# Kernel optimization log

Hardware: AMD Instinct MI355X
Metric: run time of the kernel (lower is better)

## Reference

```python
import jax, jax.numpy as jnp
import numpy as np

EMBED_DIM = 1024
NUM_HEADS = 16
HEAD_DIM = EMBED_DIM // NUM_HEADS
SCALE = HEAD_DIM ** -0.5


def setup_inputs() -> dict:
    key = jax.random.key(0)
    k1, k2, k3, k4 = jax.random.split(key, 4)
    B, N, C = 4, 2048, EMBED_DIM
    x = jax.random.normal(k1, (B, N, C), dtype=jnp.float32)
    # qkv: Linear(C, 3C, bias=False)
    w_qkv = jax.random.normal(k2, (3 * C, C), dtype=jnp.float32) * (C ** -0.5)
    # proj: Linear(C, C, bias=True)
    w_proj = jax.random.normal(k3, (C, C), dtype=jnp.float32) * (C ** -0.5)
    b_proj = jax.random.normal(k4, (C,), dtype=jnp.float32) * 0.01
    return {"x": x, "w_qkv": w_qkv, "w_proj": w_proj, "b_proj": b_proj}


def reference(x, w_qkv, w_proj, b_proj):
    B, N, C = x.shape
    H, D = NUM_HEADS, HEAD_DIM
    qkv = jnp.einsum('bnc,oc->bno', x, w_qkv)               # [B,N,3C]
    qkv = qkv.reshape(B, N, 3, H, D).transpose(2, 0, 3, 1, 4)  # [3,B,H,N,D]
    q, k, v = qkv[0], qkv[1], qkv[2]
    attn = jnp.einsum('bhnd,bhmd->bhnm', q, k) * SCALE       # [B,H,N,N]
    attn = jax.nn.softmax(attn, axis=-1)
    out = jnp.einsum('bhnm,bhmd->bhnd', attn, v)             # [B,H,N,D]
    out = out.transpose(0, 2, 1, 3).reshape(B, N, C)
    return jnp.einsum('bnc,oc->bno', out, w_proj) + b_proj
```

## Files before the change

### kernel.cpp

```cpp
#include <hip/hip_runtime.h>

#define B_ 4
#define N_ 2048
#define C_ 1024
#define H_ 16
#define D_ 64
#define M_ (B_*N_)

typedef _Float16 f16;
typedef __attribute__((ext_vector_type(2))) _Float16 f16x2;
typedef __attribute__((ext_vector_type(4))) _Float16 f16x4;
typedef __attribute__((ext_vector_type(8))) _Float16 f16x8;
typedef __attribute__((ext_vector_type(4))) float f32x4;
typedef __attribute__((ext_vector_type(16))) float f32x16;
typedef unsigned int u32;
typedef __attribute__((ext_vector_type(2))) u32 u32x2;
typedef __attribute__((ext_vector_type(4))) u32 u32x4;

__device__ __forceinline__ f32x4 mfma16(f16x8 a, f16x8 b, f32x4 c) {
  return __builtin_amdgcn_mfma_f32_16x16x32_f16(a, b, c, 0, 0, 0);
}
__device__ __forceinline__ f32x16 mfma32(f16x8 a, f16x8 b, f32x16 c) {
  return __builtin_amdgcn_mfma_f32_32x32x16_f16(a, b, c, 0, 0, 0);
}

__global__ void cast_f32_f16(const float* __restrict__ in, f16* __restrict__ out,
                             int n4, int scale_n4, float scale) {
  int i = blockIdx.x * blockDim.x + threadIdx.x;
  int stride = gridDim.x * blockDim.x;
  for (; i < n4; i += stride) {
    float4 v = reinterpret_cast<const float4*>(in)[i];
    float s = (i < scale_n4) ? scale : 1.0f;
    f16x4 o = { (f16)(v.x*s), (f16)(v.y*s), (f16)(v.z*s), (f16)(v.w*s) };
    reinterpret_cast<f16x4*>(out)[i] = o;
  }
}

template<int OUTMODE>
__global__ __launch_bounds__(256) void gemm_bt(
    const f16* __restrict__ A, const f16* __restrict__ Bm,
    f16* __restrict__ outH, float* __restrict__ outF,
    const float* __restrict__ bias, int M, int Nn, int K)
{
  __shared__ __align__(16) f16 As[128*32];
  __shared__ __align__(16) f16 Bs[128*32];
  const int tid = threadIdx.x;
  const int lane = tid & 63, wid = tid >> 6;
  const int wr = wid >> 1, wc = wid & 1;
  const int g = lane >> 4, r15 = lane & 15;
  const int nbx = Nn >> 7;
  const int cpx = gridDim.x >> 3;
  const int wg = blockIdx.x;
  const int swz = (wg & 7) * cpx + (wg >> 3);
  const int m0 = (swz / nbx) * 128, n0 = (swz % nbx) * 128;

  f32x4 acc[4][4] = {};

  for (int k0 = 0; k0 < K; k0 += 32) {
#pragma unroll
    for (int i = 0; i < 2; ++i) {
      int chunk = wid*128 + i*64 + lane;
      int row = chunk >> 2, c8 = (chunk & 3) << 3;
      const f16* ga = A  + (size_t)(m0 + row) * K + k0 + c8;
      const f16* gb = Bm + (size_t)(n0 + row) * K + k0 + c8;
      __builtin_amdgcn_global_load_lds(
        (const __attribute__((address_space(1))) unsigned int*)ga,
        (__attribute__((address_space(3))) unsigned int*)&As[(wid*128 + i*64)*8], 16, 0, 0);
      __builtin_amdgcn_global_load_lds(
        (const __attribute__((address_space(1))) unsigned int*)gb,
        (__attribute__((address_space(3))) unsigned int*)&Bs[(wid*128 + i*64)*8], 16, 0, 0);
    }
    __syncthreads();

    f16x8 af[4], bfr[4];
#pragma unroll
    for (int m = 0; m < 4; ++m)
      af[m] = *reinterpret_cast<const f16x8*>(&As[(wr*64 + m*16 + r15)*32 + g*8]);
#pragma unroll
    for (int n = 0; n < 4; ++n)
      bfr[n] = *reinterpret_cast<const f16x8*>(&Bs[(wc*64 + n*16 + r15)*32 + g*8]);
#pragma unroll
    for (int m = 0; m < 4; ++m)
#pragma unroll
      for (int n = 0; n < 4; ++n)
        acc[m][n] = mfma16(af[m], bfr[n], acc[m][n]);
    __syncthreads();
  }

#pragma unroll
  for (int m = 0; m < 4; ++m) {
#pragma unroll
    for (int n = 0; n < 4; ++n) {
#pragma unroll
      for (int r = 0; r < 4; ++r) {
        int row = m0 + wr*64 + m*16 + g*4 + r;
        int col = n0 + wc*64 + n*16 + r15;
        if (OUTMODE == 0) {
          outH[(size_t)row * Nn + col] = (f16)acc[m][n][r];
        } else {
          outF[(size_t)row * Nn + col] = acc[m][n][r] + bias[col];
        }
      }
    }
  }
}

__global__ __launch_bounds__(256) void transpose_v(const f16* __restrict__ qkv,
                                                   f16* __restrict__ vt) {
  __shared__ f16 Ts[64*64];
  const int tid = threadIdx.x;
  const int bh = blockIdx.y, b = bh >> 4, h = bh & 15;
  const int n0 = blockIdx.x * 64;
#pragma unroll
  for (int p = 0; p < 2; ++p) {
    int idx = p*256 + tid;
    int row = idx >> 3, c8 = (idx & 7) << 3;
    f16x8 v = *reinterpret_cast<const f16x8*>(
        qkv + (size_t)(b*N_ + n0 + row)*(3*C_) + 2*C_ + h*D_ + c8);
    *reinterpret_cast<f16x8*>(&Ts[row*64 + c8]) = v;
  }
  __syncthreads();
#pragma unroll
  for (int p = 0; p < 2; ++p) {
    int idx = p*256 + tid;
    int d = idx & 63, cblk = idx >> 6;
    f16x8 o;
#pragma unroll
    for (int j = 0; j < 8; ++j) o[j] = Ts[(cblk*8 + j)*64 + d];
    *reinterpret_cast<f16x8*>(vt + (size_t)(bh*64 + d)*N_ + n0 + cblk*8) = o;
  }
}

__global__ __launch_bounds__(256, 4) void attn_kernel(
    const f16* __restrict__ qkv, const f16* __restrict__ vt,
    f16* __restrict__ attn_out)
{
  __shared__ __align__(16) f16 Ks[2][64*64];
  __shared__ __align__(16) f16 Vs[2][64*64];
  const int tid = threadIdx.x;
  const int lane = tid & 63, w = tid >> 6;
  const int hi = lane >> 5;
  const int r31 = lane & 31;
  const int rm = r31 & 7;
  const int blk = blockIdx.x;
  const int xcd = blk & 7, idx = blk >> 3;
  const int bh = xcd + 8 * (idx >> 4);
  const int bx = idx & 15;
  const int b = bh >> 4, h = bh & 15;
  const int q0 = bx * 128 + w * 32;
  const int RS = 3 * C_;

  f16x8 qf[4];
  {
    const f16* qrow = qkv + (size_t)(b*N_ + q0 + r31) * RS + h*D_;
#pragma unroll
    for (int kk = 0; kk < 4; ++kk)
      qf[kk] = *reinterpret_cast<const f16x8*>(qrow + kk*16 + hi*8);
  }

  f32x16 acc0 = {}, acc1 = {};
  const f16x2 one2 = { (f16)1.0f, (f16)1.0f };
  float la = 0.f, lb = 0.f;

  int cc0 = w*64 + lane, cc1 = 256 + w*64 + lane;
  int R0 = cc0 >> 3, s0_ = (cc0 & 7) ^ (R0 & 7);
  int R1 = cc1 >> 3, s1_ = (cc1 & 7) ^ (R1 & 7);
  const f16* kg0 = qkv + (size_t)(b*N_ + R0) * RS + C_ + h*D_ + s0_*8;
  const f16* kg1 = qkv + (size_t)(b*N_ + R1) * RS + C_ + h*D_ + s1_*8;
  const f16* vg0 = vt + (size_t)(bh*D_ + R0) * N_ + s0_*8;
  const f16* vg1 = vt + (size_t)(bh*D_ + R1) * N_ + s1_*8;

  auto stage = [&](int bufi, int kv0) {
    __builtin_amdgcn_global_load_lds(
      (const __attribute__((address_space(1))) u32*)(kg0 + (size_t)kv0 * RS),
      (__attribute__((address_space(3))) u32*)&Ks[bufi][(w*64)*8], 16, 0, 0);
    __builtin_amdgcn_global_load_lds(
      (const __attribute__((address_space(1))) u32*)(kg1 + (size_t)kv0 * RS),
      (__attribute__((address_space(3))) u32*)&Ks[bufi][(256 + w*64)*8], 16, 0, 0);
    __builtin_amdgcn_global_load_lds(
      (const __attribute__((address_space(1))) u32*)(vg0 + kv0),
      (__attribute__((address_space(3))) u32*)&Vs[bufi][(w*64)*8], 16, 0, 0);
    __builtin_amdgcn_global_load_lds(
      (const __attribute__((address_space(1))) u32*)(vg1 + kv0),
      (__attribute__((address_space(3))) u32*)&Vs[bufi][(256 + w*64)*8], 16, 0, 0);
  };

  int cur = 0;
  stage(0, 0);
  __syncthreads();

  for (int it = 0; it < N_/64; ++it) {
    if (it + 1 < N_/64) stage(cur ^ 1, (it + 1) * 64);
    const f16* KsC = Ks[cur];
    const f16* VsC = Vs[cur];

#pragma unroll
    for (int hh = 0; hh < 2; ++hh) {
      f32x16 T;
      {
        const f32x16 Zc = {};
        __builtin_amdgcn_s_setprio(1);
        int ch = ((hi ^ rm) << 3);
        f16x8 k0 = *reinterpret_cast<const f16x8*>(&KsC[(hh*32 + r31)*64 + ch]);
        T = mfma32(k0, qf[0], Zc);
#pragma unroll
        for (int kk = 1; kk < 4; ++kk) {
          int ch2 = (((kk*2 + hi) ^ rm) << 3);
          f16x8 kx = *reinterpret_cast<const f16x8*>(&KsC[(hh*32 + r31)*64 + ch2]);
          T = mfma32(kx, qf[kk], T);
        }
        __builtin_amdgcn_s_setprio(0);
      }

#pragma unroll
      for (int c2 = 0; c2 < 2; ++c2) {
        float p0 = __builtin_amdgcn_exp2f(T[8*c2 + 0]);
        float p1 = __builtin_amdgcn_exp2f(T[8*c2 + 1]);
        float p2 = __builtin_amdgcn_exp2f(T[8*c2 + 2]);
        float p3 = __builtin_amdgcn_exp2f(T[8*c2 + 3]);
        float p4 = __builtin_amdgcn_exp2f(T[8*c2 + 4]);
        float p5 = __builtin_amdgcn_exp2f(T[8*c2 + 5]);
        float p6 = __builtin_amdgcn_exp2f(T[8*c2 + 6]);
        float p7 = __builtin_amdgcn_exp2f(T[8*c2 + 7]);
        u32 w0 = __builtin_bit_cast(u32, __builtin_amdgcn_cvt_pkrtz(p0, p1));
        u32 w1 = __builtin_bit_cast(u32, __builtin_amdgcn_cvt_pkrtz(p2, p3));
        u32 w2 = __builtin_bit_cast(u32, __builtin_amdgcn_cvt_pkrtz(p4, p5));
        u32 w3 = __builtin_bit_cast(u32, __builtin_amdgcn_cvt_pkrtz(p6, p7));
        la = __builtin_amdgcn_fdot2(__builtin_bit_cast(f16x2, w0), one2, la, false);
        lb = __builtin_amdgcn_fdot2(__builtin_bit_cast(f16x2, w1), one2, lb, false);
        la = __builtin_amdgcn_fdot2(__builtin_bit_cast(f16x2, w2), one2, la, false);
        lb = __builtin_amdgcn_fdot2(__builtin_bit_cast(f16x2, w3), one2, lb, false);

        u32x2 r02 = __builtin_amdgcn_permlane32_swap(w0, w2, false, false);
        u32x2 r13 = __builtin_amdgcn_permlane32_swap(w1, w3, false, false);
        u32x4 fw = { r02[0], r13[0], r02[1], r13[1] };
        f16x8 pf = __builtin_bit_cast(f16x8, fw);

        int c = hh*2 + c2;
        int ch = (((c*2 + hi) ^ rm) << 3);
        f16x8 v0 = *reinterpret_cast<const f16x8*>(&VsC[r31*64 + ch]);
        f16x8 v1 = *reinterpret_cast<const f16x8*>(&VsC[(32 + r31)*64 + ch]);
        __builtin_amdgcn_s_setprio(1);
        acc0 = mfma32(v0, pf, acc0);
        acc1 = mfma32(v1, pf, acc1);
        __builtin_amdgcn_s_setprio(0);
      }
    }

    __syncthreads();
    cur ^= 1;
  }

  float l_own = la + lb;
  float l = l_own + __shfl_xor(l_own, 32);
  float inv = 1.0f / l;
  f16* orow = attn_out + (size_t)(b*N_ + q0 + r31) * C_ + h*D_;
#pragma unroll
  for (int g2 = 0; g2 < 4; ++g2) {
    f16x4 o0, o1;
#pragma unroll
    for (int j = 0; j < 4; ++j) {
      o0[j] = (f16)(acc0[g2*4 + j] * inv);
      o1[j] = (f16)(acc1[g2*4 + j] * inv);
    }
    *reinterpret_cast<f16x4*>(orow + g2*8 + hi*4)      = o0;
    *reinterpret_cast<f16x4*>(orow + 32 + g2*8 + hi*4) = o1;
  }
}

extern "C" void kernel_launch(void* const* d_in, const int* in_sizes, int n_in,
                              void* d_out, int out_size, void* d_ws, size_t ws_size,
                              hipStream_t stream) {
  const float* x      = (const float*)d_in[0];
  const float* w_qkv  = (const float*)d_in[1];
  const float* w_proj = (const float*)d_in[2];
  const float* b_proj = (const float*)d_in[3];
  float* out = (float*)d_out;

  char* ws = (char*)d_ws;
  f16* xb     = (f16*)(ws);
  f16* wqkvb  = (f16*)(ws + 16777216);
  f16* wprojb = (f16*)(ws + 23068672);
  f16* qkvb   = (f16*)(ws + 25165824);
  f16* vtb    = (f16*)(ws + 75497472);
  f16* attnb  = xb;

  cast_f32_f16<<<2048, 256, 0, stream>>>(x,      xb,     (M_*C_)/4, 0, 1.0f);
  cast_f32_f16<<<1024, 256, 0, stream>>>(w_qkv,  wqkvb,  (3*C_*C_)/4, (C_*C_)/4, 0.18033688011112042f);
  cast_f32_f16<<<512,  256, 0, stream>>>(w_proj, wprojb, (C_*C_)/4, 0, 1.0f);

  gemm_bt<0><<<dim3((3*C_/128)*(M_/128)), 256, 0, stream>>>(
      xb, wqkvb, qkvb, nullptr, nullptr, M_, 3*C_, C_);

  transpose_v<<<dim3(N_/64, B_*H_), 256, 0, stream>>>(qkvb, vtb);

  attn_kernel<<<dim3(1024), 256, 0, stream>>>(qkvb, vtb, attnb);

  gemm_bt<1><<<dim3((C_/128)*(M_/128)), 256, 0, stream>>>(
      attnb, wprojb, nullptr, out, b_proj, M_, C_, C_);
}
```

Baseline: 221.8 us.

## Rewrite projection GEMMs with double-buffered LDS, larger tiles and swizzled layout

Replaces the single-buffered 128x128 GEMM with a 512-thread, 128x256-tile kernel that double-buffers 64-wide K slices in LDS. Loads for the next slice are issued before the MFMAs on the current one, synchronised with vmcnt waits and raw barriers. It adds an XOR swizzle on LDS columns to avoid bank conflicts, raises wave priority around the MFMA blocks, and uses supertile block swizzling for L2 reuse. The aim is to hide global-load latency and halve the number of barriers per K step. In exchange, LDS use grows to 96 KB per block and the launch grids are hardcoded, which may limit occupancy.

```diff
diff --git a/kernel.cpp b/kernel.cpp
--- a/kernel.cpp
+++ b/kernel.cpp
@@ -37,55 +37,97 @@
 }
 
 template<int OUTMODE>
-__global__ __launch_bounds__(256) void gemm_bt(
+__global__ __launch_bounds__(512, 2) void gemm_p(
     const f16* __restrict__ A, const f16* __restrict__ Bm,
     f16* __restrict__ outH, float* __restrict__ outF,
-    const float* __restrict__ bias, int M, int Nn, int K)
+    const float* __restrict__ bias, int Nn, int K, int nsup)
 {
-  __shared__ __align__(16) f16 As[128*32];
-  __shared__ __align__(16) f16 Bs[128*32];
+  __shared__ __align__(16) f16 As[2][128*64];
+  __shared__ __align__(16) f16 Bs[2][256*64];
   const int tid = threadIdx.x;
   const int lane = tid & 63, wid = tid >> 6;
-  const int wr = wid >> 1, wc = wid & 1;
+  const int wm = wid >> 2, wn = wid & 3;
   const int g = lane >> 4, r15 = lane & 15;
-  const int nbx = Nn >> 7;
-  const int cpx = gridDim.x >> 3;
-  const int wg = blockIdx.x;
-  const int swz = (wg & 7) * cpx + (wg >> 3);
-  const int m0 = (swz / nbx) * 128, n0 = (swz % nbx) * 128;
+  const int rmod = r15 & 3;
+  const int gx = (g ^ rmod) * 8;
+
+  const int s = blockIdx.x >> 4, w16 = blockIdx.x & 15;
+  const int s_swz = (s & 7) * (2 * nsup) + (s >> 3);
+  const int sm = s_swz / nsup, sn = s_swz % nsup;
+  const int m0 = (sm * 4 + (w16 >> 2)) * 128;
+  const int n0 = (sn * 4 + (w16 & 3)) * 256;
+
+  const int arow = tid >> 2, aslot = tid & 3;
+  const int akc = aslot ^ (arow & 3);
+  const f16* abase  = A  + (size_t)(m0 + arow) * K + akc * 8;
+  const f16* bbase0 = Bm + (size_t)(n0 + arow) * K + akc * 8;
+  const f16* bbase1 = Bm + (size_t)(n0 + arow + 128) * K + akc * 8;
+
+  #define STAGE(buf, kofs, kh)                                                        \
+    do {                                                                              \
+      __builtin_amdgcn_global_load_lds(                                               \
+        (const __attribute__((address_space(1))) u32*)(abase + (kofs) + (kh)*32),     \
+        (__attribute__((address_space(3))) u32*)&As[buf][(kh)*4096 + tid*8], 16,0,0); \
+      __builtin_amdgcn_global_load_lds(                                               \
+        (const __attribute__((address_space(1))) u32*)(bbase0 + (kofs) + (kh)*32),    \
+        (__attribute__((address_space(3))) u32*)&Bs[buf][(kh)*8192 + tid*8], 16,0,0); \
+      __builtin_amdgcn_global_load_lds(                                               \
+        (const __attribute__((address_space(1))) u32*)(bbase1 + (kofs) + (kh)*32),    \
+        (__attribute__((address_space(3))) u32*)&Bs[buf][(kh)*8192 + (tid+512)*8], 16,0,0); \
+    } while (0)
 
   f32x4 acc[4][4] = {};
-
-  for (int k0 = 0; k0 < K; k0 += 32) {
-#pragma unroll
-    for (int i = 0; i < 2; ++i) {
-      int chunk = wid*128 + i*64 + lane;
-      int row = chunk >> 2, c8 = (chunk & 3) << 3;
-      const f16* ga = A  + (size_t)(m0 + row) * K + k0 + c8;
-      const f16* gb = Bm + (size_t)(n0 + row) * K + k0 + c8;
-      __builtin_amdgcn_global_load_lds(
-        (const __attribute__((address_space(1))) unsigned int*)ga,
-        (__attribute__((address_space(3))) unsigned int*)&As[(wid*128 + i*64)*8], 16, 0, 0);
-      __builtin_amdgcn_global_load_lds(
-        (const __attribute__((address_space(1))) unsigned int*)gb,
-        (__attribute__((address_space(3))) unsigned int*)&Bs[(wid*128 + i*64)*8], 16, 0, 0);
+  const int nt = K / 64;
+
+  STAGE(0, 0, 0);
+  STAGE(0, 0, 1);
+
+  int cur = 0;
+  for (int t = 0; t < nt - 1; ++t) {
+#pragma unroll
+    for (int kk = 0; kk < 2; ++kk) {
+      asm volatile("s_waitcnt vmcnt(3)" ::: "memory");
+      __builtin_amdgcn_s_barrier();
+      STAGE(cur ^ 1, (t + 1) * 64, kk);
+      f16x8 af[4], bf[4];
+#pragma unroll
+      for (int m = 0; m < 4; ++m)
+        af[m] = *reinterpret_cast<const f16x8*>(&As[cur][kk*4096 + (wm*64 + m*16 + r15)*32 + gx]);
+#pragma unroll
+      for (int n = 0; n < 4; ++n)
+        bf[n] = *reinterpret_cast<const f16x8*>(&Bs[cur][kk*8192 + (wn*64 + n*16 + r15)*32 + gx]);
+      __builtin_amdgcn_s_setprio(1);
+#pragma unroll
+      for (int m = 0; m < 4; ++m)
+#pragma unroll
+        for (int n = 0; n < 4; ++n)
+          acc[m][n] = mfma16(af[m], bf[n], acc[m][n]);
+      __builtin_amdgcn_s_setprio(0);
     }
-    __syncthreads();
-
-    f16x8 af[4], bfr[4];
+    cur ^= 1;
+  }
+
+#pragma unroll
+  for (int kk = 0; kk < 2; ++kk) {
+    if (kk == 0) asm volatile("s_waitcnt vmcnt(3)" ::: "memory");
+    else         asm volatile("s_waitcnt vmcnt(0)" ::: "memory");
+    __builtin_amdgcn_s_barrier();
+    f16x8 af[4], bf[4];
 #pragma unroll
     for (int m = 0; m < 4; ++m)
-      af[m] = *reinterpret_cast<const f16x8*>(&As[(wr*64 + m*16 + r15)*32 + g*8]);
+      af[m] = *reinterpret_cast<const f16x8*>(&As[cur][kk*4096 + (wm*64 + m*16 + r15)*32 + gx]);
 #pragma unroll
     for (int n = 0; n < 4; ++n)
-      bfr[n] = *reinterpret_cast<const f16x8*>(&Bs[(wc*64 + n*16 + r15)*32 + g*8]);
+      bf[n] = *reinterpret_cast<const f16x8*>(&Bs[cur][kk*8192 + (wn*64 + n*16 + r15)*32 + gx]);
+    __builtin_amdgcn_s_setprio(1);
 #pragma unroll
     for (int m = 0; m < 4; ++m)
 #pragma unroll
       for (int n = 0; n < 4; ++n)
-        acc[m][n] = mfma16(af[m], bfr[n], acc[m][n]);
-    __syncthreads();
-  }
+        acc[m][n] = mfma16(af[m], bf[n], acc[m][n]);
+    __builtin_amdgcn_s_setprio(0);
+  }
+  #undef STAGE
 
 #pragma unroll
   for (int m = 0; m < 4; ++m) {
@@ -93,8 +135,8 @@
     for (int n = 0; n < 4; ++n) {
 #pragma unroll
       for (int r = 0; r < 4; ++r) {
-        int row = m0 + wr*64 + m*16 + g*4 + r;
-        int col = n0 + wc*64 + n*16 + r15;
+        int row = m0 + wm*64 + m*16 + g*4 + r;
+        int col = n0 + wn*64 + n*16 + r15;
         if (OUTMODE == 0) {
           outH[(size_t)row * Nn + col] = (f16)acc[m][n][r];
         } else {
@@ -289,13 +331,13 @@
   cast_f32_f16<<<1024, 256, 0, stream>>>(w_qkv,  wqkvb,  (3*C_*C_)/4, (C_*C_)/4, 0.18033688011112042f);
   cast_f32_f16<<<512,  256, 0, stream>>>(w_proj, wprojb, (C_*C_)/4, 0, 1.0f);
 
-  gemm_bt<0><<<dim3((3*C_/128)*(M_/128)), 256, 0, stream>>>(
-      xb, wqkvb, qkvb, nullptr, nullptr, M_, 3*C_, C_);
+  gemm_p<0><<<dim3(768), 512, 0, stream>>>(
+      xb, wqkvb, qkvb, nullptr, nullptr, 3*C_, C_, 3);
 
   transpose_v<<<dim3(N_/64, B_*H_), 256, 0, stream>>>(qkvb, vtb);
 
   attn_kernel<<<dim3(1024), 256, 0, stream>>>(qkvb, vtb, attnb);
 
-  gemm_bt<1><<<dim3((C_/128)*(M_/128)), 256, 0, stream>>>(
-      attnb, wprojb, nullptr, out, b_proj, M_, C_, C_);
-}
+  gemm_p<1><<<dim3(256), 512, 0, stream>>>(
+      attnb, wprojb, nullptr, out, b_proj, C_, C_, 1);
+}
```

Result: slower. 240.9 us (+8.7%).
